# Kernel tuning notes

Hardware: AMD Instinct MI355X
Metric: run time of the kernel (lower is better)

## Reference

```python
import jax, jax.numpy as jnp
import numpy as np

B, L, D_TOK, N_HEAD, D_QK, D_V, TOPK = 4, 1024, 897, 8, 512, 768, 8
NEG = -10000.0


def setup_inputs() -> dict:
    key = jax.random.key(0)
    ks = jax.random.split(key, 8)
    q = jax.random.normal(ks[0], (B, L, D_TOK), jnp.float32)
    k = jax.random.normal(ks[1], (B, L, D_TOK), jnp.float32)
    v = jax.random.normal(ks[2], (B, L, D_V), jnp.float32)
    # self-patch exclusion mask (registered buffer 10000*eye, applied negatively)
    qk_mask = NEG * jnp.eye(L, dtype=jnp.float32)[None, None]  # [1,1,L,L]
    k_mask = jax.random.normal(ks[3], (B, 1, L, 1), jnp.float32)  # additive key mask
    w_qs = jax.random.normal(ks[4], (D_TOK, N_HEAD * D_QK), jnp.float32) / np.sqrt(D_TOK)
    w_ks = jax.random.normal(ks[5], (D_TOK, N_HEAD * D_QK), jnp.float32) / np.sqrt(D_TOK)
    w_vs = jax.random.normal(ks[6], (D_V, N_HEAD * D_V), jnp.float32) / np.sqrt(D_V)
    w_fc = jax.random.normal(ks[7], (N_HEAD * D_V, D_V), jnp.float32) / np.sqrt(N_HEAD * D_V)
    return {"q": q, "k": k, "v": v, "qk_mask": qk_mask, "k_mask": k_mask,
            "w_qs": w_qs, "w_ks": w_ks, "w_vs": w_vs, "w_fc": w_fc}


def _topk_sparsify(attn):
    # keep top-k scores per query row, set the rest to -10000 (exact torch scatter semantics)
    vals, idx = jax.lax.top_k(attn, TOPK)                      # [B,H,L,TOPK]
    flat = jnp.full((B * N_HEAD * L, L), NEG, attn.dtype)
    rows = jnp.arange(B * N_HEAD * L)[:, None]
    flat = flat.at[rows, idx.reshape(-1, TOPK)].set(vals.reshape(-1, TOPK))
    return flat.reshape(B, N_HEAD, L, L)


def reference(q, k, v, qk_mask, k_mask, w_qs, w_ks, w_vs, w_fc):
    # projections -> [B, H, L, d]
    qh = (q @ w_qs).reshape(B, L, N_HEAD, D_QK).transpose(0, 2, 1, 3)
    kh = (k @ w_ks).reshape(B, L, N_HEAD, D_QK).transpose(0, 2, 1, 3)
    vh = (v @ w_vs).reshape(B, L, N_HEAD, D_V).transpose(0, 2, 1, 3)
    scale = 1.0 / jnp.sqrt(jnp.asarray(D_QK, qh.dtype))
    attn = jnp.einsum('bhqd,bhkd->bhqk', qh * scale, kh)
    attn = attn + qk_mask + k_mask[..., 0][:, :, None, :]      # k_mask.squeeze(-1).unsqueeze(-2)
    attn = _topk_sparsify(attn)
    attn = jax.nn.softmax(attn.astype(jnp.float32), axis=-1).astype(v.dtype)
    out = jnp.einsum('bhqk,bhkd->bhqd', attn, vh)              # [B,H,L,d_v]
    out = out.transpose(0, 2, 1, 3).reshape(B, L, N_HEAD * D_V)
    out = out @ w_fc                                           # [B,L,d_v]; add_residual=False, dropout eval
    return out, attn
```

## Files before the change

### kernel.cpp

```cpp
#include <hip/hip_runtime.h>
#include <math.h>

#define NB 4
#define NL 1024
#define NDT 897
#define NH 8
#define NDQ 512
#define NDV 768
#define NTOP 8
#define NCAND 16
#define KP 928
#define SCALE 0.044194173824159216

typedef unsigned short ushort_t;
typedef __attribute__((ext_vector_type(8))) short short8;
typedef __attribute__((ext_vector_type(4))) float f32x4;

static __device__ __forceinline__ ushort_t f2bf(float f) {
    unsigned u = __float_as_uint(f);
    unsigned r = (u + 0x7fffu + ((u >> 16) & 1u)) >> 16;
    return (ushort_t)r;
}
static __device__ __forceinline__ float bf2f(ushort_t u) {
    return __uint_as_float((unsigned)u << 16);
}
static __device__ __forceinline__ void split3(float x, ushort_t& b1, ushort_t& b2, ushort_t& b3) {
    b1 = f2bf(x);
    float r1 = x - bf2f(b1);
    b2 = f2bf(r1);
    float r2 = r1 - bf2f(b2);
    b3 = f2bf(r2);
}

__global__ __launch_bounds__(256)
void split_w(const float* __restrict__ w_qs, const float* __restrict__ w_ks,
             ushort_t* __restrict__ wsp)
{
    const float* W = (blockIdx.z == 0) ? w_qs : w_ks;
    ushort_t* dst = wsp + (size_t)blockIdx.z * 3 * 4096 * KP;
    const int n0 = blockIdx.x * 64;
    const int k0 = blockIdx.y * 32;
    __shared__ float tf[32][65];
    const int t = threadIdx.x;
#pragma unroll
    for (int it = 0; it < 8; it++) {
        int kk = it * 4 + (t >> 6);
        int nn = t & 63;
        int kg = k0 + kk;
        tf[kk][nn] = (kg < NDT) ? W[(size_t)kg * 4096 + n0 + nn] : 0.f;
    }
    __syncthreads();
    const int nn = t >> 2;
    const int oct = t & 3;
    ushort_t o[3][8];
#pragma unroll
    for (int j = 0; j < 8; j++) {
        float x = tf[oct * 8 + j][nn];
        split3(x, o[0][j], o[1][j], o[2][j]);
    }
#pragma unroll
    for (int p = 0; p < 3; p++)
        *(uint4*)(dst + ((size_t)p * 4096 + n0 + nn) * KP + k0 + oct * 8) = *(const uint4*)o[p];
}

__global__ __launch_bounds__(256)
void split_a(const float* __restrict__ q, const float* __restrict__ k,
             ushort_t* __restrict__ asp, int b)
{
    const int row = blockIdx.x;
    const int z = blockIdx.y;
    const float* A = (z == 0 ? q : k) + ((size_t)b * NL + row) * NDT;
    ushort_t* dst = asp + (size_t)z * 3 * 1024 * KP;
    const int t = threadIdx.x;
    if (t >= 232) return;
    const int kb = t * 4;
    ushort_t o[3][4];
#pragma unroll
    for (int j = 0; j < 4; j++) {
        int kk = kb + j;
        float x = (kk < NDT) ? A[kk] : 0.f;
        split3(x, o[0][j], o[1][j], o[2][j]);
    }
#pragma unroll
    for (int p = 0; p < 3; p++)
        *(uint2*)(dst + ((size_t)p * 1024 + row) * KP + kb) = *(const uint2*)o[p];
}

__global__ __launch_bounds__(256)
void proj_qk_mfma6(const ushort_t* __restrict__ asp, const ushort_t* __restrict__ wsp,
                   float* __restrict__ qh32, float* __restrict__ kh32,
                   ushort_t* __restrict__ qhb, ushort_t* __restrict__ khb)
{
    const int z = blockIdx.z;
    const int n0 = blockIdx.x * 128, m0 = blockIdx.y * 128;
    float*    C32 = z == 0 ? qh32 : kh32;
    ushort_t* Cb  = z == 0 ? qhb  : khb;
    const ushort_t* Ab = asp + (size_t)z * 3 * 1024 * KP;
    const ushort_t* Bb = wsp + (size_t)z * 3 * 4096 * KP;

    __shared__ ushort_t Al[3 * 128 * 40];
    __shared__ ushort_t Bl[3 * 128 * 40];
    const int t = threadIdx.x;
    const int lane = t & 63, wv = t >> 6;
    const int quad = lane >> 4, l16 = lane & 15;

    f32x4 acc[2][8];
#pragma unroll
    for (int i = 0; i < 2; i++)
#pragma unroll
        for (int j = 0; j < 8; j++) acc[i][j] = (f32x4){0.f, 0.f, 0.f, 0.f};

    for (int kc = 0; kc < KP; kc += 32) {
#pragma unroll
        for (int p = 0; p < 3; p++) {
            const ushort_t* Ap = Ab + (size_t)p * 1024 * KP;
            const ushort_t* Bp = Bb + (size_t)p * 4096 * KP;
#pragma unroll
            for (int pp = 0; pp < 2; pp++) {
                int c = t + pp * 256;
                int r = c >> 2, ck = c & 3;
                int pc = (ck + ((r + (r >> 3)) & 3)) & 3;
                uint4 va = *(const uint4*)(Ap + (size_t)(m0 + r) * KP + kc + ck * 8);
                *(uint4*)&Al[p * 5120 + r * 40 + pc * 8] = va;
                uint4 vb = *(const uint4*)(Bp + (size_t)(n0 + r) * KP + kc + ck * 8);
                *(uint4*)&Bl[p * 5120 + r * 40 + pc * 8] = vb;
            }
        }
        __syncthreads();

        short8 af[3][2], bf[3][8];
#pragma unroll
        for (int p = 0; p < 3; p++) {
#pragma unroll
            for (int i = 0; i < 2; i++) {
                int r = wv * 32 + i * 16 + l16;
                int pc = (quad + ((r + (r >> 3)) & 3)) & 3;
                af[p][i] = *(const short8*)&Al[p * 5120 + r * 40 + pc * 8];
            }
#pragma unroll
            for (int j = 0; j < 8; j++) {
                int r = j * 16 + l16;
                int pc = (quad + ((r + (r >> 3)) & 3)) & 3;
                bf[p][j] = *(const short8*)&Bl[p * 5120 + r * 40 + pc * 8];
            }
        }
#pragma unroll
        for (int i = 0; i < 2; i++)
#pragma unroll
            for (int j = 0; j < 8; j++) {
                acc[i][j] = __builtin_amdgcn_mfma_f32_16x16x32_bf16(af[0][i], bf[0][j], acc[i][j], 0, 0, 0);
                acc[i][j] = __builtin_amdgcn_mfma_f32_16x16x32_bf16(af[0][i], bf[1][j], acc[i][j], 0, 0, 0);
                acc[i][j] = __builtin_amdgcn_mfma_f32_16x16x32_bf16(af[1][i], bf[0][j], acc[i][j], 0, 0, 0);
                acc[i][j] = __builtin_amdgcn_mfma_f32_16x16x32_bf16(af[0][i], bf[2][j], acc[i][j], 0, 0, 0);
                acc[i][j] = __builtin_amdgcn_mfma_f32_16x16x32_bf16(af[1][i], bf[1][j], acc[i][j], 0, 0, 0);
                acc[i][j] = __builtin_amdgcn_mfma_f32_16x16x32_bf16(af[2][i], bf[0][j], acc[i][j], 0, 0, 0);
            }
        __syncthreads();
    }

#pragma unroll
    for (int i = 0; i < 2; i++)
#pragma unroll
        for (int j = 0; j < 8; j++) {
            int gn = n0 + j * 16 + l16;
#pragma unroll
            for (int reg = 0; reg < 4; reg++) {
                int gm = m0 + wv * 32 + i * 16 + quad * 4 + reg;
                float vv = acc[i][j][reg];
                C32[(size_t)gm * 4096 + gn] = vv;
                Cb[(size_t)gm * 4096 + gn] = f2bf(vv);
            }
        }
}

__global__ __launch_bounds__(256)
void scores_mfma(const ushort_t* __restrict__ qhb, const ushort_t* __restrict__ khb,
                 const float* __restrict__ kmask, float* __restrict__ sc, int b)
{
    const int h = blockIdx.z;
    const int n0 = blockIdx.x * 128, m0 = blockIdx.y * 128;
    __shared__ ushort_t Al[128 * 40];
    __shared__ ushort_t Bl[128 * 40];
    const int t = threadIdx.x;
    const int lane = t & 63, wv = t >> 6;
    const int quad = lane >> 4, l16 = lane & 15;

    f32x4 acc[2][8];
#pragma unroll
    for (int i = 0; i < 2; i++)
#pragma unroll
        for (int j = 0; j < 8; j++) acc[i][j] = (f32x4){0.f, 0.f, 0.f, 0.f};

    const ushort_t* Ag = qhb + (size_t)h * NDQ;
    const ushort_t* Bg = khb + (size_t)h * NDQ;

    for (int kc = 0; kc < NDQ; kc += 32) {
#pragma unroll
        for (int p = 0; p < 2; p++) {
            int c = t + p * 256;
            int r = c >> 2, ck = c & 3;
            int pc = (ck + ((r + (r >> 3)) & 3)) & 3;
            uint4 va = *(const uint4*)(Ag + (size_t)(m0 + r) * 4096 + kc + ck * 8);
            *(uint4*)&Al[r * 40 + pc * 8] = va;
        }
#pragma unroll
        for (int p = 0; p < 2; p++) {
            int c = t + p * 256;
            int r = c >> 2, ck = c & 3;
            int pc = (ck + ((r + (r >> 3)) & 3)) & 3;
            uint4 vb = *(const uint4*)(Bg + (size_t)(n0 + r) * 4096 + kc + ck * 8);
            *(uint4*)&Bl[r * 40 + pc * 8] = vb;
        }
        __syncthreads();

        short8 af[2], bf[8];
#pragma unroll
        for (int i = 0; i < 2; i++) {
            int r = wv * 32 + i * 16 + l16;
            int pc = (quad + ((r + (r >> 3)) & 3)) & 3;
            af[i] = *(const short8*)&Al[r * 40 + pc * 8];
        }
#pragma unroll
        for (int j = 0; j < 8; j++) {
            int r = j * 16 + l16;
            int pc = (quad + ((r + (r >> 3)) & 3)) & 3;
            bf[j] = *(const short8*)&Bl[r * 40 + pc * 8];
        }
#pragma unroll
        for (int i = 0; i < 2; i++)
#pragma unroll
            for (int j = 0; j < 8; j++)
                acc[i][j] = __builtin_amdgcn_mfma_f32_16x16x32_bf16(af[i], bf[j], acc[i][j], 0, 0, 0);
        __syncthreads();
    }

    const float scl = (float)SCALE;
#pragma unroll
    for (int i = 0; i < 2; i++) {
#pragma unroll
        for (int j = 0; j < 8; j++) {
            int gn = n0 + j * 16 + l16;
            float km = kmask[b * NL + gn];
#pragma unroll
            for (int reg = 0; reg < 4; reg++) {
                int gm = m0 + wv * 32 + i * 16 + quad * 4 + reg;
                float s = acc[i][j][reg] * scl + km;
                if (gm == gn) s -= 10000.0f;
                sc[((size_t)h * NL + gm) * NL + gn] = s;
            }
        }
    }
}

__global__ __launch_bounds__(256)
void select_rescore(float* __restrict__ sc,
                    const float* __restrict__ qh32, const float* __restrict__ kh32,
                    const float* __restrict__ kmask,
                    float* __restrict__ topw, int* __restrict__ topi, int b)
{
    const int lane = threadIdx.x & 63;
    const int w = threadIdx.x >> 6;
    const int r = blockIdx.x * 4 + w;
    const int q = r & 1023, h = r >> 10;

    float* row = sc + (size_t)r * NL;
    float v[16];
#pragma unroll
    for (int j = 0; j < 16; j++) v[j] = row[lane + 64 * j];

    {
        float4 z = make_float4(0.f, 0.f, 0.f, 0.f);
#pragma unroll
        for (int p = 0; p < 4; p++)
            *(float4*)(row + p * 256 + lane * 4) = z;
    }

    int cidx[NCAND];
    for (int tsel = 0; tsel < NCAND; tsel++) {
        float bv = v[0]; int bj = 0;
#pragma unroll
        for (int j = 1; j < 16; j++)
            if (v[j] > bv) { bv = v[j]; bj = j; }
        int bi = lane + 64 * bj;
#pragma unroll
        for (int s = 1; s < 64; s <<= 1) {
            float ov = __shfl_xor(bv, s);
            int   oi = __shfl_xor(bi, s);
            if (ov > bv || (ov == bv && oi < bi)) { bv = ov; bi = oi; }
        }
        cidx[tsel] = bi;
        bool own = (lane == (bi & 63));
        int jj = bi >> 6;
#pragma unroll
        for (int j = 0; j < 16; j++)
            if (own && j == jj) v[j] = -3.0e38f;
    }

    const float* qrow  = qh32 + (size_t)q * 4096 + h * NDQ;
    const float* kbase = kh32 + h * NDQ;
    double qd[8];
#pragma unroll
    for (int j = 0; j < 8; j++) qd[j] = (double)qrow[lane + 64 * j];

    double sv[NCAND]; int si[NCAND];
#pragma unroll
    for (int c = 0; c < NCAND; c++) {
        int idx = cidx[c];
        const float* krow = kbase + (size_t)idx * 4096;
        double s = 0.0;
#pragma unroll
        for (int j = 0; j < 8; j++) s = fma(qd[j], (double)krow[lane + 64 * j], s);
#pragma unroll
        for (int sh = 1; sh < 64; sh <<= 1) s += __shfl_xor(s, sh);
        s = s * SCALE + (double)kmask[b * NL + idx];
        if (idx == q) s -= 10000.0;
        sv[c] = s; si[c] = idx;
    }
    double vs[NTOP]; int is_[NTOP];
    unsigned used = 0;
#pragma unroll
    for (int tsel = 0; tsel < NTOP; tsel++) {
        double bv = -1.0e300; int bi = 1 << 30; int bc = 0;
#pragma unroll
        for (int c = 0; c < NCAND; c++) {
            bool free_c = !(used & (1u << c));
            bool better = free_c && (sv[c] > bv || (sv[c] == bv && si[c] < bi));
            if (better) { bv = sv[c]; bi = si[c]; bc = c; }
        }
        used |= (1u << bc);
        vs[tsel] = bv; is_[tsel] = bi;
    }
    double m = vs[0];
    double e[NTOP], Z = 0.0;
#pragma unroll
    for (int i = 0; i < NTOP; i++) { e[i] = exp(vs[i] - m); Z += e[i]; }

    __asm__ volatile("s_waitcnt vmcnt(0)" ::: "memory");

    if (lane == 0) {
#pragma unroll
        for (int i = 0; i < NTOP; i++) {
            float wv = (float)(e[i] / Z);
            topw[(size_t)r * NTOP + i] = wv;
            topi[(size_t)r * NTOP + i] = is_[i];
            row[is_[i]] = wv;
        }
    }
}

__global__ __launch_bounds__(256)
void combine_M(const float* __restrict__ w_vs, const float* __restrict__ w_fc,
               ushort_t* __restrict__ MhTb)
{
    const int h = blockIdx.z;
    const int K = NDV;
    __shared__ float As[16][68];
    __shared__ float Bs[16][68];
    const int t = threadIdx.x;
    const int tx = t & 15, ty = t >> 4;
    const int m0 = blockIdx.x * 64, n0 = blockIdx.y * 64;

    float acc[4][4];
#pragma unroll
    for (int i = 0; i < 4; i++)
#pragma unroll
        for (int j = 0; j < 4; j++) acc[i][j] = 0.f;

    for (int k0 = 0; k0 < K; k0 += 16) {
        {
            int am = t >> 2;
            int a4 = (t & 3) * 4;
            float4 v = *(const float4*)(w_vs + (size_t)(m0 + am) * (NH * NDV) + h * NDV + k0 + a4);
            As[a4 + 0][am] = v.x; As[a4 + 1][am] = v.y;
            As[a4 + 2][am] = v.z; As[a4 + 3][am] = v.w;
        }
        {
            int bk = t >> 4;
            int bn = (t & 15) * 4;
            float4 v = *(const float4*)(w_fc + (size_t)(h * NDV + k0 + bk) * NDV + n0 + bn);
            Bs[bk][bn + 0] = v.x; Bs[bk][bn + 1] = v.y;
            Bs[bk][bn + 2] = v.z; Bs[bk][bn + 3] = v.w;
        }
        __syncthreads();
#pragma unroll
        for (int kk = 0; kk < 16; kk++) {
            float a[4], bb[4];
#pragma unroll
            for (int i = 0; i < 4; i++) {
                a[i]  = As[kk][ty * 4 + i];
                bb[i] = Bs[kk][tx * 4 + i];
            }
#pragma unroll
            for (int i = 0; i < 4; i++)
#pragma unroll
                for (int j = 0; j < 4; j++)
                    acc[i][j] = fmaf(a[i], bb[j], acc[i][j]);
        }
        __syncthreads();
    }
#pragma unroll
    for (int i = 0; i < 4; i++) {
        int gm = m0 + ty * 4 + i;
#pragma unroll
        for (int j = 0; j < 4; j++) {
            int gn = n0 + tx * 4 + j;
            MhTb[((size_t)h * NDV + gn) * NDV + gm] = f2bf(acc[i][j]);
        }
    }
}

__global__ __launch_bounds__(256)
void conv_v_bf16(const float* __restrict__ v, ushort_t* __restrict__ vb)
{
    size_t i = ((size_t)blockIdx.x * 256 + threadIdx.x) * 4;
    float4 f = *(const float4*)(v + i);
    ushort_t o[4] = { f2bf(f.x), f2bf(f.y), f2bf(f.z), f2bf(f.w) };
    *(uint2*)(vb + i) = *(uint2*)o;
}

__global__ __launch_bounds__(256)
void vw_mfma(const ushort_t* __restrict__ vb, const ushort_t* __restrict__ MhTb,
             float* __restrict__ vw, int b)
{
    const int h = blockIdx.z;
    const int n0 = blockIdx.x * 128, m0 = blockIdx.y * 128;
    __shared__ ushort_t Al[128 * 40];
    __shared__ ushort_t Bl[128 * 40];
    const int t = threadIdx.x;
    const int lane = t & 63, wv = t >> 6;
    const int quad = lane >> 4, l16 = lane & 15;

    f32x4 acc[2][8];
#pragma unroll
    for (int i = 0; i < 2; i++)
#pragma unroll
        for (int j = 0; j < 8; j++) acc[i][j] = (f32x4){0.f, 0.f, 0.f, 0.f};

    const ushort_t* Ag = vb + (size_t)b * NL * NDV;
    const ushort_t* Bg = MhTb + (size_t)h * NDV * NDV;

    for (int kc = 0; kc < NDV; kc += 32) {
#pragma unroll
        for (int p = 0; p < 2; p++) {
            int c = t + p * 256;
            int r = c >> 2, ck = c & 3;
            int pc = (ck + ((r + (r >> 3)) & 3)) & 3;
            uint4 va = *(const uint4*)(Ag + (size_t)(m0 + r) * NDV + kc + ck * 8);
            *(uint4*)&Al[r * 40 + pc * 8] = va;
        }
#pragma unroll
        for (int p = 0; p < 2; p++) {
            int c = t + p * 256;
            int r = c >> 2, ck = c & 3;
            int pc = (ck + ((r + (r >> 3)) & 3)) & 3;
            uint4 vv = *(const uint4*)(Bg + (size_t)(n0 + r) * NDV + kc + ck * 8);
            *(uint4*)&Bl[r * 40 + pc * 8] = vv;
        }
        __syncthreads();

        short8 af[2], bf[8];
#pragma unroll
        for (int i = 0; i < 2; i++) {
            int r = wv * 32 + i * 16 + l16;
            int pc = (quad + ((r + (r >> 3)) & 3)) & 3;
            af[i] = *(const short8*)&Al[r * 40 + pc * 8];
        }
#pragma unroll
        for (int j = 0; j < 8; j++) {
            int r = j * 16 + l16;
            int pc = (quad + ((r + (r >> 3)) & 3)) & 3;
            bf[j] = *(const short8*)&Bl[r * 40 + pc * 8];
        }
#pragma unroll
        for (int i = 0; i < 2; i++)
#pragma unroll
            for (int j = 0; j < 8; j++)
                acc[i][j] = __builtin_amdgcn_mfma_f32_16x16x32_bf16(af[i], bf[j], acc[i][j], 0, 0, 0);
        __syncthreads();
    }

#pragma unroll
    for (int i = 0; i < 2; i++) {
#pragma unroll
        for (int j = 0; j < 8; j++) {
            int gn = n0 + j * 16 + l16;
#pragma unroll
            for (int reg = 0; reg < 4; reg++) {
                int gm = m0 + wv * 32 + i * 16 + quad * 4 + reg;
                vw[((size_t)h * NL + gm) * NDV + gn] = acc[i][j][reg];
            }
        }
    }
}

__global__ __launch_bounds__(256)
void gather_out(const float* __restrict__ vw, const float* __restrict__ topw,
                const int* __restrict__ topi, float* __restrict__ out, int b)
{
    const int q = blockIdx.x;
    __shared__ float sw[64];
    __shared__ int   sidx[64];
    const int t = threadIdx.x;
    if (t < 64) {
        int h = t >> 3, i = t & 7;
        size_t rr = ((size_t)h * NL + q) * NTOP + i;
        sw[t]   = topw[rr];
        sidx[t] = topi[rr] + h * NL;
    }
    __syncthreads();
    float* orow = out + (size_t)(b * NL + q) * NDV;
    for (int dv = t; dv < NDV; dv += 256) {
        float acc = 0.f;
#pragma unroll
        for (int j = 0; j < 64; j++)
            acc = fmaf(sw[j], vw[(size_t)sidx[j] * NDV + dv], acc);
        orow[dv] = acc;
    }
}

extern "C" void kernel_launch(void* const* d_in, const int* in_sizes, int n_in,
                              void* d_out, int out_size, void* d_ws, size_t ws_size,
                              hipStream_t stream)
{
    const float* q     = (const float*)d_in[0];
    const float* k     = (const float*)d_in[1];
    const float* v     = (const float*)d_in[2];
    const float* kmask = (const float*)d_in[4];
    const float* w_qs  = (const float*)d_in[5];
    const float* w_ks  = (const float*)d_in[6];
    const float* w_vs  = (const float*)d_in[7];
    const float* w_fc  = (const float*)d_in[8];

    char* ws = (char*)d_ws;
    float*    qh32 = (float*)   (ws + 0);
    float*    kh32 = (float*)   (ws + 16777216);
    ushort_t* qhb  = (ushort_t*)(ws + 33554432);
    ushort_t* khb  = (ushort_t*)(ws + 41943040);
    ushort_t* MhTb = (ushort_t*)(ws + 50331648);
    ushort_t* vb16 = (ushort_t*)(ws + 59768832);
    float*    topw = (float*)   (ws + 66060288);
    int*      topi = (int*)     (ws + 66322432);
    ushort_t* wsp  = (ushort_t*)(ws + 66584576);
    ushort_t* asp  = (ushort_t*)(ws + 112197632);
    float*    vw   = (float*)   (ws + 0);

    float* out  = (float*)d_out;
    float* attn = out + (size_t)NB * NL * NDV;

    split_w    <<<dim3(64, 29, 2), 256, 0, stream>>>(w_qs, w_ks, wsp);
    combine_M  <<<dim3(12, 12, 8), 256, 0, stream>>>(w_vs, w_fc, MhTb);
    conv_v_bf16<<<3072, 256, 0, stream>>>(v, vb16);

    for (int b = 0; b < NB; b++) {
        float* slab = attn + (size_t)b * NH * NL * NL;

        split_a       <<<dim3(1024, 2), 256, 0, stream>>>(q, k, asp, b);
        proj_qk_mfma6 <<<dim3(32, 8, 2), 256, 0, stream>>>(asp, wsp, qh32, kh32, qhb, khb);
        scores_mfma   <<<dim3(8, 8, 8), 256, 0, stream>>>(qhb, khb, kmask, slab, b);
        select_rescore<<<2048, 256, 0, stream>>>(slab, qh32, kh32, kmask, topw, topi, b);
        vw_mfma       <<<dim3(6, 8, 8), 256, 0, stream>>>(vb16, MhTb, vw, b);
        gather_out    <<<NL, 256, 0, stream>>>(vw, topw, topi, out, b);
    }
}
```

Measured before the change: 1.473 ms.

## Compute combined value/output weight product with split-bf16 MFMA instead of FP32 FMA

Replaces the scalar FP32 tiled GEMM that forms the per-head product of w_vs and w_fc with an MFMA kernel. Both operands are first split into two bf16 parts (hi and lo) and multiplied with three MFMA products, which roughly preserves fp32 accuracy. The split buffers reuse the weight-split workspace region, so split_w is now launched after the combine kernel. This adds two preprocessing kernels and extra memory traffic in exchange for much higher matrix throughput on the 8x768x768x768 product.

```diff
diff --git a/kernel.cpp b/kernel.cpp
--- a/kernel.cpp
+++ b/kernel.cpp
@@ -31,6 +31,10 @@
     float r2 = r1 - bf2f(b2);
     b3 = f2bf(r2);
 }
+static __device__ __forceinline__ void split2(float x, ushort_t& b1, ushort_t& b2) {
+    b1 = f2bf(x);
+    b2 = f2bf(x - bf2f(b1));
+}
 
 __global__ __launch_bounds__(256)
 void split_w(const float* __restrict__ w_qs, const float* __restrict__ w_ks,
@@ -61,6 +65,125 @@
 #pragma unroll
     for (int p = 0; p < 3; p++)
         *(uint4*)(dst + ((size_t)p * 4096 + n0 + nn) * KP + k0 + oct * 8) = *(const uint4*)o[p];
+}
+
+__global__ __launch_bounds__(256)
+void split_wvs(const float* __restrict__ w_vs, ushort_t* __restrict__ wvs2)
+{
+    int gid8 = ((int)blockIdx.x * 256 + threadIdx.x) * 8;
+    int dk  = gid8 / 6144;
+    int rem = gid8 % 6144;
+    int h   = rem / 768;
+    int kk  = rem % 768;
+    const float* src = w_vs + (size_t)dk * 6144 + rem;
+    ushort_t o[2][8];
+#pragma unroll
+    for (int j = 0; j < 8; j++) split2(src[j], o[0][j], o[1][j]);
+#pragma unroll
+    for (int p = 0; p < 2; p++)
+        *(uint4*)(wvs2 + ((size_t)(p * 8 + h) * 768 + dk) * 768 + kk) = *(const uint4*)o[p];
+}
+
+__global__ __launch_bounds__(256)
+void split_wfcT(const float* __restrict__ w_fc, ushort_t* __restrict__ wfcT2)
+{
+    const int dv0 = blockIdx.x * 64;
+    const int kg0 = blockIdx.y * 32;
+    __shared__ float tf[32][65];
+    const int t = threadIdx.x;
+#pragma unroll
+    for (int it = 0; it < 8; it++) {
+        int kk = it * 4 + (t >> 6);
+        int dd = t & 63;
+        tf[kk][dd] = w_fc[(size_t)(kg0 + kk) * 768 + dv0 + dd];
+    }
+    __syncthreads();
+    const int dv = t >> 2;
+    const int oct = t & 3;
+    const int h  = kg0 / 768;
+    const int kl = kg0 % 768;
+    ushort_t o[2][8];
+#pragma unroll
+    for (int j = 0; j < 8; j++) split2(tf[oct * 8 + j][dv], o[0][j], o[1][j]);
+#pragma unroll
+    for (int p = 0; p < 2; p++)
+        *(uint4*)(wfcT2 + ((size_t)(p * 8 + h) * 768 + dv0 + dv) * 768 + kl + oct * 8) = *(const uint4*)o[p];
+}
+
+__global__ __launch_bounds__(256)
+void combine_mfma(const ushort_t* __restrict__ wfcT2, const ushort_t* __restrict__ wvs2,
+                  ushort_t* __restrict__ MhTb)
+{
+    const int h = blockIdx.z;
+    const int n0 = blockIdx.x * 128, m0 = blockIdx.y * 128;
+    __shared__ ushort_t Al[2 * 5120];
+    __shared__ ushort_t Bl[2 * 5120];
+    const int t = threadIdx.x;
+    const int lane = t & 63, wv = t >> 6;
+    const int quad = lane >> 4, l16 = lane & 15;
+
+    f32x4 acc[2][8];
+#pragma unroll
+    for (int i = 0; i < 2; i++)
+#pragma unroll
+        for (int j = 0; j < 8; j++) acc[i][j] = (f32x4){0.f, 0.f, 0.f, 0.f};
+
+    for (int kc = 0; kc < 768; kc += 32) {
+#pragma unroll
+        for (int p = 0; p < 2; p++) {
+            const ushort_t* Ap = wfcT2 + (size_t)(p * 8 + h) * 768 * 768;
+            const ushort_t* Bp = wvs2  + (size_t)(p * 8 + h) * 768 * 768;
+#pragma unroll
+            for (int pp = 0; pp < 2; pp++) {
+                int c = t + pp * 256;
+                int r = c >> 2, ck = c & 3;
+                int pc = (ck + ((r + (r >> 3)) & 3)) & 3;
+                uint4 va = *(const uint4*)(Ap + (size_t)(m0 + r) * 768 + kc + ck * 8);
+                *(uint4*)&Al[p * 5120 + r * 40 + pc * 8] = va;
+                uint4 vb = *(const uint4*)(Bp + (size_t)(n0 + r) * 768 + kc + ck * 8);
+                *(uint4*)&Bl[p * 5120 + r * 40 + pc * 8] = vb;
+            }
+        }
+        __syncthreads();
+
+        short8 af[2][2], bf[2][8];
+#pragma unroll
+        for (int p = 0; p < 2; p++) {
+#pragma unroll
+            for (int i = 0; i < 2; i++) {
+                int r = wv * 32 + i * 16 + l16;
+                int pc = (quad + ((r + (r >> 3)) & 3)) & 3;
+                af[p][i] = *(const short8*)&Al[p * 5120 + r * 40 + pc * 8];
+            }
+#pragma unroll
+            for (int j = 0; j < 8; j++) {
+                int r = j * 16 + l16;
+                int pc = (quad + ((r + (r >> 3)) & 3)) & 3;
+                bf[p][j] = *(const short8*)&Bl[p * 5120 + r * 40 + pc * 8];
+            }
+        }
+#pragma unroll
+        for (int i = 0; i < 2; i++)
+#pragma unroll
+            for (int j = 0; j < 8; j++) {
+                acc[i][j] = __builtin_amdgcn_mfma_f32_16x16x32_bf16(af[0][i], bf[0][j], acc[i][j], 0, 0, 0);
+                acc[i][j] = __builtin_amdgcn_mfma_f32_16x16x32_bf16(af[0][i], bf[1][j], acc[i][j], 0, 0, 0);
+                acc[i][j] = __builtin_amdgcn_mfma_f32_16x16x32_bf16(af[1][i], bf[0][j], acc[i][j], 0, 0, 0);
+            }
+        __syncthreads();
+    }
+
+#pragma unroll
+    for (int i = 0; i < 2; i++)
+#pragma unroll
+        for (int j = 0; j < 8; j++) {
+            int gn = n0 + j * 16 + l16;
+#pragma unroll
+            for (int reg = 0; reg < 4; reg++) {
+                int gm = m0 + wv * 32 + i * 16 + quad * 4 + reg;
+                MhTb[((size_t)h * NDV + gm) * NDV + gn] = f2bf(acc[i][j][reg]);
+            }
+        }
 }
 
 __global__ __launch_bounds__(256)
@@ -344,67 +467,6 @@
             topw[(size_t)r * NTOP + i] = wv;
             topi[(size_t)r * NTOP + i] = is_[i];
             row[is_[i]] = wv;
-        }
-    }
-}
-
-__global__ __launch_bounds__(256)
-void combine_M(const float* __restrict__ w_vs, const float* __restrict__ w_fc,
-               ushort_t* __restrict__ MhTb)
-{
-    const int h = blockIdx.z;
-    const int K = NDV;
-    __shared__ float As[16][68];
-    __shared__ float Bs[16][68];
-    const int t = threadIdx.x;
-    const int tx = t & 15, ty = t >> 4;
-    const int m0 = blockIdx.x * 64, n0 = blockIdx.y * 64;
-
-    float acc[4][4];
-#pragma unroll
-    for (int i = 0; i < 4; i++)
-#pragma unroll
-        for (int j = 0; j < 4; j++) acc[i][j] = 0.f;
-
-    for (int k0 = 0; k0 < K; k0 += 16) {
-        {
-            int am = t >> 2;
-            int a4 = (t & 3) * 4;
-            float4 v = *(const float4*)(w_vs + (size_t)(m0 + am) * (NH * NDV) + h * NDV + k0 + a4);
-            As[a4 + 0][am] = v.x; As[a4 + 1][am] = v.y;
-            As[a4 + 2][am] = v.z; As[a4 + 3][am] = v.w;
-        }
-        {
-            int bk = t >> 4;
-            int bn = (t & 15) * 4;
-            float4 v = *(const float4*)(w_fc + (size_t)(h * NDV + k0 + bk) * NDV + n0 + bn);
-            Bs[bk][bn + 0] = v.x; Bs[bk][bn + 1] = v.y;
-            Bs[bk][bn + 2] = v.z; Bs[bk][bn + 3] = v.w;
-        }
-        __syncthreads();
-#pragma unroll
-        for (int kk = 0; kk < 16; kk++) {
-            float a[4], bb[4];
-#pragma unroll
-            for (int i = 0; i < 4; i++) {
-                a[i]  = As[kk][ty * 4 + i];
-                bb[i] = Bs[kk][tx * 4 + i];
-            }
-#pragma unroll
-            for (int i = 0; i < 4; i++)
-#pragma unroll
-                for (int j = 0; j < 4; j++)
-                    acc[i][j] = fmaf(a[i], bb[j], acc[i][j]);
-        }
-        __syncthreads();
-    }
-#pragma unroll
-    for (int i = 0; i < 4; i++) {
-        int gm = m0 + ty * 4 + i;
-#pragma unroll
-        for (int j = 0; j < 4; j++) {
-            int gn = n0 + tx * 4 + j;
-            MhTb[((size_t)h * NDV + gn) * NDV + gm] = f2bf(acc[i][j]);
         }
     }
 }
@@ -543,13 +605,17 @@
     ushort_t* wsp  = (ushort_t*)(ws + 66584576);
     ushort_t* asp  = (ushort_t*)(ws + 112197632);
     float*    vw   = (float*)   (ws + 0);
+    ushort_t* wfcT2 = (ushort_t*)(ws + 66584576);
+    ushort_t* wvs2  = (ushort_t*)(ws + 66584576 + 18874368);
 
     float* out  = (float*)d_out;
     float* attn = out + (size_t)NB * NL * NDV;
 
-    split_w    <<<dim3(64, 29, 2), 256, 0, stream>>>(w_qs, w_ks, wsp);
-    combine_M  <<<dim3(12, 12, 8), 256, 0, stream>>>(w_vs, w_fc, MhTb);
-    conv_v_bf16<<<3072, 256, 0, stream>>>(v, vb16);
+    split_wvs   <<<2304, 256, 0, stream>>>(w_vs, wvs2);
+    split_wfcT  <<<dim3(12, 192), 256, 0, stream>>>(w_fc, wfcT2);
+    combine_mfma<<<dim3(6, 6, 8), 256, 0, stream>>>(wfcT2, wvs2, MhTb);
+    split_w     <<<dim3(64, 29, 2), 256, 0, stream>>>(w_qs, w_ks, wsp);
+    conv_v_bf16 <<<3072, 256, 0, stream>>>(v, vb16);
 
     for (int b = 0; b < NB; b++) {
         float* slab = attn + (size_t)b * NH * NL * NL;
```

New measurement: 1.439 ms. 2.3% less time.
